# Performance work log

Hardware: AMD Instinct MI355X
Metric: run time of the kernel (lower is better)

The kernel has to match this reference:

```python
import jax, jax.numpy as jnp
import numpy as np

B, L, P, NH = 16384, 64, 2, 128
T = L // P          # number of patches (GRU steps)
NOUT = 1 << P       # softmax over 2**p possible patches


def setup_inputs() -> dict:
    key = jax.random.key(0)
    ks = jax.random.split(key, 10)
    s_in = 1.0 / np.sqrt(NH)
    x = jax.random.randint(ks[0], (B, L, 1), 0, 2).astype(jnp.float32)
    return {
        "x": x,
        # GRU params, torch layout: gates ordered (r, z, n)
        "w_ih": jax.random.normal(ks[1], (3 * NH, P), jnp.float32) * s_in,
        "w_hh": jax.random.normal(ks[2], (3 * NH, NH), jnp.float32) * s_in,
        "b_ih": jax.random.normal(ks[3], (3 * NH,), jnp.float32) * s_in,
        "b_hh": jax.random.normal(ks[4], (3 * NH,), jnp.float32) * s_in,
        # MLP head: Linear(Nh,Nh) -> ReLU -> Linear(Nh, 2**p) -> Softmax
        "w1": jax.random.normal(ks[5], (NH, NH), jnp.float32) * s_in,
        "b1": jax.random.normal(ks[6], (NH,), jnp.float32) * s_in,
        "w2": jax.random.normal(ks[7], (NOUT, NH), jnp.float32) * s_in,
        "b2": jax.random.normal(ks[8], (NOUT,), jnp.float32) * s_in,
    }


def _gru_mlp_logp(x, w_ih, w_hh, b_ih, b_hh, w1, b1, w2, b2):
    b = x.shape[0]
    patches = x.reshape(b, T, P)                       # Patch1D.forward
    # shift right by one patch (teacher forcing input), first step is zeros
    data = jnp.concatenate([jnp.zeros((b, 1, P), x.dtype), patches[:, :-1]], axis=1)
    # precompute all input-side gate projections: [B,T,3*Nh]
    xi = jnp.einsum('btp,gp->btg', data, w_ih) + b_ih

    def step(h, xi_t):
        gi_r, gi_z, gi_n = jnp.split(xi_t, 3, axis=-1)
        gh = h @ w_hh.T + b_hh
        gh_r, gh_z, gh_n = jnp.split(gh, 3, axis=-1)
        r = jax.nn.sigmoid(gi_r + gh_r)
        z = jax.nn.sigmoid(gi_z + gh_z)
        n = jnp.tanh(gi_n + r * gh_n)
        h_new = (1.0 - z) * n + z * h
        return h_new, h_new

    h0 = jnp.zeros((b, NH), x.dtype)
    _, hs = jax.lax.scan(step, h0, jnp.swapaxes(xi, 0, 1))  # [T,B,Nh]
    hs = jnp.swapaxes(hs, 0, 1)                              # [B,T,Nh]

    hid = jax.nn.relu(hs @ w1.T + b1)
    probs = jax.nn.softmax(hid @ w2.T + b2, axis=-1)         # [B,T,2**p]

    # genpatch2onehot: binary-encode each patch, little-endian (bit i -> 2**i)
    weights = (1 << jnp.arange(P)).astype(jnp.float32)
    idx = jnp.sum(patches * weights, axis=-1).astype(jnp.int32)  # [B,T]
    total = jnp.take_along_axis(probs, idx[..., None], axis=-1)[..., 0]
    return jnp.sum(jnp.log(total), axis=1)                   # [B]


def reference(x, w_ih, w_hh, b_ih, b_hh, w1, b1, w2, b2):
    return _gru_mlp_logp(x, w_ih, w_hh, b_ih, b_hh, w1, b1, w2, b2)
```

## Files before the change

kernel.cpp:

```cpp
#include <hip/hip_runtime.h>
#include <hip/hip_bf16.h>


#define NSTEP 32
#define BT    32
#define BLK   512

using s8v = __attribute__((ext_vector_type(8))) short;
using f4v = __attribute__((ext_vector_type(4))) float;

#define L2E 1.4426950408889634f
#define LN2 0.6931471805599453f

__device__ __forceinline__ unsigned short f2bf(float f) {
  __hip_bfloat16 h = __float2bfloat16(f);
  return __builtin_bit_cast(unsigned short, h);
}
__device__ __forceinline__ unsigned pkbf2(float a, float b) {
  return (unsigned)f2bf(a) | ((unsigned)f2bf(b) << 16);
}
__device__ __forceinline__ s8v pack8(float4 u, float4 v) {
  s8v a;
  a[0]=(short)f2bf(u.x); a[1]=(short)f2bf(u.y); a[2]=(short)f2bf(u.z); a[3]=(short)f2bf(u.w);
  a[4]=(short)f2bf(v.x); a[5]=(short)f2bf(v.y); a[6]=(short)f2bf(v.z); a[7]=(short)f2bf(v.w);
  return a;
}
__device__ __forceinline__ f4v mfma16(s8v a, s8v b, f4v c) {
  return __builtin_amdgcn_mfma_f32_16x16x32_bf16(a, b, c, 0, 0, 0);
}
__device__ __forceinline__ float sigm(float x) {
  return __builtin_amdgcn_rcpf(1.f + __builtin_amdgcn_exp2f(-L2E * x));
}
__device__ __forceinline__ float tanhc(float x) {
  return __builtin_fmaf(2.f, __builtin_amdgcn_rcpf(1.f + __builtin_amdgcn_exp2f((-2.f*L2E) * x)), -1.f);
}

__global__ __launch_bounds__(BLK, 4) void prnn_kernel(
    const float* __restrict__ x, const float* __restrict__ w_ih,
    const float* __restrict__ w_hh, const float* __restrict__ b_ih,
    const float* __restrict__ b_hh, const float* __restrict__ w1,
    const float* __restrict__ b1, const float* __restrict__ w2,
    const float* __restrict__ b2, float* __restrict__ out) {

  __shared__ __align__(16) unsigned char lds_h[4*2*64*16];
  __shared__ __align__(16) unsigned char lds_hid[4*2*64*16];
  __shared__ __align__(16) unsigned char lds_wA1[8*4*64*16];
  __shared__ __align__(16) unsigned char lds_w2f[4*64*16];
  __shared__ __align__(16) float lds_xrz[64*4*4];
  __shared__ __align__(16) float lds_xn[32*4*4];
  __shared__ __align__(16) float lds_bb[256];
  __shared__ __align__(16) float lds_b2[4];
  __shared__ unsigned lds_idx[32*8];
  __shared__ float lds_lp[8][32];

  const int tid = threadIdx.x;
  const int bbase = blockIdx.x * BT;
  const int lane = tid & 63;
  const int lg = lane >> 4, ln = lane & 15;
  const int w = __builtin_amdgcn_readfirstlane(tid >> 6);

  if (tid < 256) {
    int b = tid >> 3, ch = tid & 7;
    const float* xp = x + (size_t)(bbase + b) * 64 + ch * 8;
    float4 v0 = *(const float4*)xp, v1 = *(const float4*)(xp + 4);
    unsigned pk = ((v0.x!=0.f?1u:0u) | (v0.y!=0.f?2u:0u))
               | (((v0.z!=0.f?1u:0u) | (v0.w!=0.f?2u:0u)) << 8)
               | (((v1.x!=0.f?1u:0u) | (v1.y!=0.f?2u:0u)) << 16)
               | (((v1.z!=0.f?1u:0u) | (v1.w!=0.f?2u:0u)) << 24);
    lds_idx[b*8 + ch] = pk;
  }
  if (tid < 256) {
    int j = tid;
    float base = b_ih[j] + b_hh[j];
    float wa = w_ih[2*j], wb = w_ih[2*j+1];
    int q = j >> 2, e = j & 3;
    #pragma unroll
    for (int v = 0; v < 4; ++v)
      lds_xrz[(q*4+v)*4 + e] = base + ((v&1) ? wa : 0.f) + ((v&2) ? wb : 0.f);
  }
  if (tid < 128) {
    int j2 = 256 + tid;
    float bn = b_ih[j2];
    float wan = w_ih[2*j2], wbn = w_ih[2*j2+1];
    int qn = tid >> 2, en = tid & 3;
    #pragma unroll
    for (int v = 0; v < 4; ++v)
      lds_xn[(qn*4+v)*4 + en] = bn + ((v&1) ? wan : 0.f) + ((v&2) ? wbn : 0.f);
  }
  if (tid < 128) lds_bb[tid] = b_hh[256 + tid];
  else if (tid < 256) lds_bb[tid] = b1[tid - 128];
  if (tid < 4) lds_b2[tid] = b2[tid];
  #pragma unroll
  for (int it = 0; it < 4; ++it) {
    int i = tid + it * BLK;
    int mt = i >> 8, ks = (i >> 6) & 3, l = i & 63;
    const float* src = w1 + (16*mt + (l & 15)) * 128 + ks*32 + (l >> 4)*8;
    *(s8v*)(lds_wA1 + ((mt*4 + ks)*64 + l)*16) = pack8(*(const float4*)src, *(const float4*)(src+4));
  }
  if (tid < 256) {
    int ks = tid >> 6, l = tid & 63;
    s8v fr;
    #pragma unroll
    for (int e = 0; e < 8; ++e) fr[e] = (short)0;
    if ((l & 15) < 4) {
      const float* src = w2 + (l & 15) * 128 + ks*32 + (l >> 4)*8;
      fr = pack8(*(const float4*)src, *(const float4*)(src + 4));
    }
    *(s8v*)(lds_w2f + (ks*64 + l)*16) = fr;
  }

  s8v Ar[4], Az[4], An[4];
  {
    const int row = 16*w + ln;
    #pragma unroll
    for (int ks = 0; ks < 4; ++ks) {
      const float* s0 = w_hh + row*128 + ks*32 + lg*8;
      Ar[ks] = pack8(*(const float4*)s0, *(const float4*)(s0 + 4));
      const float* s1 = s0 + 128*128;
      Az[ks] = pack8(*(const float4*)s1, *(const float4*)(s1 + 4));
      const float* s2 = s0 + 256*128;
      An[ks] = pack8(*(const float4*)s2, *(const float4*)(s2 + 4));
    }
  }

  __syncthreads();

  unsigned pk0a=0, pk0b=0, pk1a=0, pk1b=0;
  #pragma unroll
  for (int w8 = 0; w8 < 4; ++w8) {
    unsigned u = lds_idx[ln*8 + w8];
    pk0a |= (((u&3u) | ((u>>6)&0xCu) | ((u>>12)&0x30u) | ((u>>18)&0xC0u)) << (8*w8));
    unsigned u2 = lds_idx[(16+ln)*8 + w8];
    pk1a |= (((u2&3u) | ((u2>>6)&0xCu) | ((u2>>12)&0x30u) | ((u2>>18)&0xC0u)) << (8*w8));
  }
  #pragma unroll
  for (int w8 = 4; w8 < 8; ++w8) {
    unsigned u = lds_idx[ln*8 + w8];
    pk0b |= (((u&3u) | ((u>>6)&0xCu) | ((u>>12)&0x30u) | ((u>>18)&0xC0u)) << (8*(w8-4)));
    unsigned u2 = lds_idx[(16+ln)*8 + w8];
    pk1b |= (((u2&3u) | ((u2>>6)&0xCu) | ((u2>>12)&0x30u) | ((u2>>18)&0xC0u)) << (8*(w8-4)));
  }

  const unsigned wroff = (unsigned)((((w>>1)*128) + 16*(2*(w&1) + (lg>>1)) + ln)*16 + 8*(lg&1));
  const int q = 4*w + lg;

  s8v Bf[4][2];
  #pragma unroll
  for (int ks = 0; ks < 4; ++ks)
    #pragma unroll
    for (int nt = 0; nt < 2; ++nt)
      #pragma unroll
      for (int e = 0; e < 8; ++e) Bf[ks][nt][e] = (short)0;
  f4v hfr[2];
  hfr[0][0]=0.f; hfr[0][1]=0.f; hfr[0][2]=0.f; hfr[0][3]=0.f;
  hfr[1] = hfr[0];
  float lp0 = 0.f, lp1 = 0.f;
  int pv0 = 0, pv1 = 0;

  for (int tb = 0; tb < NSTEP; tb += 8) {
    const unsigned pc0 = (tb & 16) ? pk0b : pk0a;
    const unsigned pc1 = (tb & 16) ? pk1b : pk1a;
    #pragma unroll
    for (int k = 0; k < 8; ++k) {
      const int t = tb + k;
      const f4v aNi = *(const f4v*)&lds_bb[q*4];
      #pragma unroll
      for (int nt = 0; nt < 2; ++nt) {
        const int var = nt ? pv1 : pv0;
        f4v aR = *(const f4v*)&lds_xrz[(q*4 + var)*4];
        f4v aZ = *(const f4v*)&lds_xrz[((q+32)*4 + var)*4];
        f4v aN = aNi;
        #pragma unroll
        for (int ks = 0; ks < 4; ++ks) {
          aR = mfma16(Ar[ks], Bf[ks][nt], aR);
          aZ = mfma16(Az[ks], Bf[ks][nt], aZ);
          aN = mfma16(An[ks], Bf[ks][nt], aN);
        }
        const f4v xnv = *(const f4v*)&lds_xn[(q*4 + var)*4];
        f4v hn;
        #pragma unroll
        for (int r = 0; r < 4; ++r) {
          float R  = sigm(aR[r]);
          float Z  = sigm(aZ[r]);
          float Ng = tanhc(__builtin_fmaf(R, aN[r], xnv[r]));
          hn[r] = __builtin_fmaf(Z, hfr[nt][r] - Ng, Ng);
        }
        hfr[nt] = hn;
        uint2 wv;
        wv.x = pkbf2(hn[0], hn[1]);
        wv.y = pkbf2(hn[2], hn[3]);
        *(uint2*)(lds_h + wroff + (unsigned)(nt*1024)) = wv;
      }
      __syncthreads();
      #pragma unroll
      for (int ks = 0; ks < 4; ++ks)
        #pragma unroll
        for (int nt = 0; nt < 2; ++nt)
          Bf[ks][nt] = *(const s8v*)(lds_h + ((ks*2 + nt)*64 + lane)*16);
      const f4v b1i = *(const f4v*)&lds_bb[128 + q*4];
      f4v hc0 = b1i, hc1 = b1i;
      #pragma unroll
      for (int ks = 0; ks < 4; ++ks) {
        const s8v wf = *(const s8v*)(lds_wA1 + ((w*4 + ks)*64 + lane)*16);
        hc0 = mfma16(wf, Bf[ks][0], hc0);
        hc1 = mfma16(wf, Bf[ks][1], hc1);
      }
      {
        uint2 wv;
        wv.x = pkbf2(fmaxf(hc0[0],0.f), fmaxf(hc0[1],0.f));
        wv.y = pkbf2(fmaxf(hc0[2],0.f), fmaxf(hc0[3],0.f));
        *(uint2*)(lds_hid + wroff) = wv;
        wv.x = pkbf2(fmaxf(hc1[0],0.f), fmaxf(hc1[1],0.f));
        wv.y = pkbf2(fmaxf(hc1[2],0.f), fmaxf(hc1[3],0.f));
        *(uint2*)(lds_hid + wroff + 1024u) = wv;
      }
      __syncthreads();
      const int sh  = (2*t) & 31;
      const int ic0 = (int)((pc0 >> sh) & 3);
      const int ic1 = (int)((pc1 >> sh) & 3);
      if (w == k) {
        const f4v b2v = *(const f4v*)lds_b2;
        f4v la0, la1;
        #pragma unroll
        for (int r = 0; r < 4; ++r) {
          la0[r] = (lg == 0) ? b2v[r] : 0.f;
          la1[r] = la0[r];
        }
        #pragma unroll
        for (int ks = 0; ks < 4; ++ks) {
          const s8v W2f = *(const s8v*)(lds_w2f + (ks*64 + lane)*16);
          la0 = mfma16(W2f, *(const s8v*)(lds_hid + ((ks*2 + 0)*64 + lane)*16), la0);
          la1 = mfma16(W2f, *(const s8v*)(lds_hid + ((ks*2 + 1)*64 + lane)*16), la1);
        }
        if (lg == 0) {
          {
            float l0=la0[0], l1=la0[1], l2=la0[2], l3=la0[3];
            float m = fmaxf(fmaxf(l0, l1), fmaxf(l2, l3));
            float s = __builtin_amdgcn_exp2f((l0-m)*L2E) + __builtin_amdgcn_exp2f((l1-m)*L2E)
                    + __builtin_amdgcn_exp2f((l2-m)*L2E) + __builtin_amdgcn_exp2f((l3-m)*L2E);
            float sel = (ic0 == 0) ? l0 : (ic0 == 1) ? l1 : (ic0 == 2) ? l2 : l3;
            lp0 += (sel - m) - __builtin_amdgcn_logf(s) * LN2;
          }
          {
            float l0=la1[0], l1=la1[1], l2=la1[2], l3=la1[3];
            float m = fmaxf(fmaxf(l0, l1), fmaxf(l2, l3));
            float s = __builtin_amdgcn_exp2f((l0-m)*L2E) + __builtin_amdgcn_exp2f((l1-m)*L2E)
                    + __builtin_amdgcn_exp2f((l2-m)*L2E) + __builtin_amdgcn_exp2f((l3-m)*L2E);
            float sel = (ic1 == 0) ? l0 : (ic1 == 1) ? l1 : (ic1 == 2) ? l2 : l3;
            lp1 += (sel - m) - __builtin_amdgcn_logf(s) * LN2;
          }
        }
      }
      pv0 = ic0; pv1 = ic1;
    }
  }

  if (lg == 0) { lds_lp[w][ln] = lp0; lds_lp[w][16 + ln] = lp1; }
  __syncthreads();
  if (tid < 32) {
    float s = 0.f;
    #pragma unroll
    for (int ww = 0; ww < 8; ++ww) s += lds_lp[ww][tid];
    out[bbase + tid] = s;
  }
}

extern "C" void kernel_launch(void* const* d_in, const int* in_sizes, int n_in,
                              void* d_out, int out_size, void* d_ws, size_t ws_size,
                              hipStream_t stream) {
  const float* x    = (const float*)d_in[0];
  const float* w_ih = (const float*)d_in[1];
  const float* w_hh = (const float*)d_in[2];
  const float* b_ih = (const float*)d_in[3];
  const float* b_hh = (const float*)d_in[4];
  const float* w1   = (const float*)d_in[5];
  const float* b1   = (const float*)d_in[6];
  const float* w2   = (const float*)d_in[7];
  const float* b2   = (const float*)d_in[8];
  float* out = (float*)d_out;
  int B = in_sizes[0] / 64;
  int grid = B / BT;
  prnn_kernel<<<grid, BLK, 0, stream>>>(x, w_ih, w_hh, b_ih, b_hh, w1, b1, w2, b2, out);
}
```

Before: 100.0 us.

## Double-buffer GRU hidden/MLP LDS to drop a barrier and defer the output head

```diff
diff --git a/kernel.cpp b/kernel.cpp
--- a/kernel.cpp
+++ b/kernel.cpp
@@ -19,20 +19,20 @@
 __device__ __forceinline__ unsigned pkbf2(float a, float b) {
   return (unsigned)f2bf(a) | ((unsigned)f2bf(b) << 16);
 }
-__device__ __forceinline__ s8v pack8(float4 u, float4 v) {
+__device__ __forceinline__ s8v pack8s(float sc, float4 u, float4 v) {
   s8v a;
-  a[0]=(short)f2bf(u.x); a[1]=(short)f2bf(u.y); a[2]=(short)f2bf(u.z); a[3]=(short)f2bf(u.w);
-  a[4]=(short)f2bf(v.x); a[5]=(short)f2bf(v.y); a[6]=(short)f2bf(v.z); a[7]=(short)f2bf(v.w);
+  a[0]=(short)f2bf(sc*u.x); a[1]=(short)f2bf(sc*u.y); a[2]=(short)f2bf(sc*u.z); a[3]=(short)f2bf(sc*u.w);
+  a[4]=(short)f2bf(sc*v.x); a[5]=(short)f2bf(sc*v.y); a[6]=(short)f2bf(sc*v.z); a[7]=(short)f2bf(sc*v.w);
   return a;
 }
 __device__ __forceinline__ f4v mfma16(s8v a, s8v b, f4v c) {
   return __builtin_amdgcn_mfma_f32_16x16x32_bf16(a, b, c, 0, 0, 0);
 }
-__device__ __forceinline__ float sigm(float x) {
-  return __builtin_amdgcn_rcpf(1.f + __builtin_amdgcn_exp2f(-L2E * x));
-}
-__device__ __forceinline__ float tanhc(float x) {
-  return __builtin_fmaf(2.f, __builtin_amdgcn_rcpf(1.f + __builtin_amdgcn_exp2f((-2.f*L2E) * x)), -1.f);
+__device__ __forceinline__ float sigm2(float x) {
+  return __builtin_amdgcn_rcpf(1.f + __builtin_amdgcn_exp2f(-x));
+}
+__device__ __forceinline__ float tanh2(float x) {
+  return __builtin_fmaf(2.f, __builtin_amdgcn_rcpf(1.f + __builtin_amdgcn_exp2f(-x)), -1.f);
 }
 
 __global__ __launch_bounds__(BLK, 4) void prnn_kernel(
@@ -42,14 +42,12 @@
     const float* __restrict__ b1, const float* __restrict__ w2,
     const float* __restrict__ b2, float* __restrict__ out) {
 
-  __shared__ __align__(16) unsigned char lds_h[4*2*64*16];
-  __shared__ __align__(16) unsigned char lds_hid[4*2*64*16];
+  __shared__ __align__(16) unsigned char lds_h[2][8192];
+  __shared__ __align__(16) unsigned char lds_hid[2][8192];
   __shared__ __align__(16) unsigned char lds_wA1[8*4*64*16];
   __shared__ __align__(16) unsigned char lds_w2f[4*64*16];
   __shared__ __align__(16) float lds_xrz[64*4*4];
   __shared__ __align__(16) float lds_xn[32*4*4];
-  __shared__ __align__(16) float lds_bb[256];
-  __shared__ __align__(16) float lds_b2[4];
   __shared__ unsigned lds_idx[32*8];
   __shared__ float lds_lp[8][32];
 
@@ -76,7 +74,7 @@
     int q = j >> 2, e = j & 3;
     #pragma unroll
     for (int v = 0; v < 4; ++v)
-      lds_xrz[(q*4+v)*4 + e] = base + ((v&1) ? wa : 0.f) + ((v&2) ? wb : 0.f);
+      lds_xrz[(q*4+v)*4 + e] = L2E * (base + ((v&1) ? wa : 0.f) + ((v&2) ? wb : 0.f));
   }
   if (tid < 128) {
     int j2 = 256 + tid;
@@ -85,17 +83,14 @@
     int qn = tid >> 2, en = tid & 3;
     #pragma unroll
     for (int v = 0; v < 4; ++v)
-      lds_xn[(qn*4+v)*4 + en] = bn + ((v&1) ? wan : 0.f) + ((v&2) ? wbn : 0.f);
-  }
-  if (tid < 128) lds_bb[tid] = b_hh[256 + tid];
-  else if (tid < 256) lds_bb[tid] = b1[tid - 128];
-  if (tid < 4) lds_b2[tid] = b2[tid];
+      lds_xn[(qn*4+v)*4 + en] = (2.f*L2E) * (bn + ((v&1) ? wan : 0.f) + ((v&2) ? wbn : 0.f));
+  }
   #pragma unroll
   for (int it = 0; it < 4; ++it) {
     int i = tid + it * BLK;
     int mt = i >> 8, ks = (i >> 6) & 3, l = i & 63;
     const float* src = w1 + (16*mt + (l & 15)) * 128 + ks*32 + (l >> 4)*8;
-    *(s8v*)(lds_wA1 + ((mt*4 + ks)*64 + l)*16) = pack8(*(const float4*)src, *(const float4*)(src+4));
+    *(s8v*)(lds_wA1 + ((mt*4 + ks)*64 + l)*16) = pack8s(1.f, *(const float4*)src, *(const float4*)(src+4));
   }
   if (tid < 256) {
     int ks = tid >> 6, l = tid & 63;
@@ -104,7 +99,7 @@
     for (int e = 0; e < 8; ++e) fr[e] = (short)0;
     if ((l & 15) < 4) {
       const float* src = w2 + (l & 15) * 128 + ks*32 + (l >> 4)*8;
-      fr = pack8(*(const float4*)src, *(const float4*)(src + 4));
+      fr = pack8s(1.f, *(const float4*)src, *(const float4*)(src + 4));
     }
     *(s8v*)(lds_w2f + (ks*64 + l)*16) = fr;
   }
@@ -115,12 +110,21 @@
     #pragma unroll
     for (int ks = 0; ks < 4; ++ks) {
       const float* s0 = w_hh + row*128 + ks*32 + lg*8;
-      Ar[ks] = pack8(*(const float4*)s0, *(const float4*)(s0 + 4));
+      Ar[ks] = pack8s(L2E, *(const float4*)s0, *(const float4*)(s0 + 4));
       const float* s1 = s0 + 128*128;
-      Az[ks] = pack8(*(const float4*)s1, *(const float4*)(s1 + 4));
+      Az[ks] = pack8s(L2E, *(const float4*)s1, *(const float4*)(s1 + 4));
       const float* s2 = s0 + 256*128;
-      An[ks] = pack8(*(const float4*)s2, *(const float4*)(s2 + 4));
-    }
+      An[ks] = pack8s(2.f*L2E, *(const float4*)s2, *(const float4*)(s2 + 4));
+    }
+  }
+  const int q = 4*w + lg;
+  f4v bhnr, b1i, b2r;
+  {
+    const f4v bh = *(const f4v*)(b_hh + 256 + q*4);
+    bhnr[0]=(2.f*L2E)*bh[0]; bhnr[1]=(2.f*L2E)*bh[1]; bhnr[2]=(2.f*L2E)*bh[2]; bhnr[3]=(2.f*L2E)*bh[3];
+    b1i = *(const f4v*)(b1 + q*4);
+    if (lg == 0) b2r = *(const f4v*)b2;
+    else { b2r[0]=0.f; b2r[1]=0.f; b2r[2]=0.f; b2r[3]=0.f; }
   }
 
   __syncthreads();
@@ -142,7 +146,6 @@
   }
 
   const unsigned wroff = (unsigned)((((w>>1)*128) + 16*(2*(w&1) + (lg>>1)) + ln)*16 + 8*(lg&1));
-  const int q = 4*w + lg;
 
   s8v Bf[4][2];
   #pragma unroll
@@ -157,19 +160,43 @@
   float lp0 = 0.f, lp1 = 0.f;
   int pv0 = 0, pv1 = 0;
 
+  auto do_p5 = [&](int u, int uslot) {
+    const int ua = u & 7;
+    const bool d0 = (w == ua), d1 = (w == (ua ^ 4));
+    if (d0 | d1) {
+      const int ntx = d1 ? 1 : 0;
+      f4v la = b2r;
+      #pragma unroll
+      for (int ks = 0; ks < 4; ++ks) {
+        const s8v W2f = *(const s8v*)(lds_w2f + (ks*64 + lane)*16);
+        const s8v Bh  = *(const s8v*)(&lds_hid[uslot][((ks*2 + ntx)*64 + lane)*16]);
+        la = mfma16(W2f, Bh, la);
+      }
+      if (lg == 0) {
+        const unsigned hsel = ntx ? ((u & 16) ? pk1b : pk1a) : ((u & 16) ? pk0b : pk0a);
+        const int ic = (int)((hsel >> ((2*u) & 31)) & 3);
+        float l0=la[0], l1=la[1], l2=la[2], l3=la[3];
+        float m = fmaxf(fmaxf(l0, l1), fmaxf(l2, l3));
+        float s = __builtin_amdgcn_exp2f((l0-m)*L2E) + __builtin_amdgcn_exp2f((l1-m)*L2E)
+                + __builtin_amdgcn_exp2f((l2-m)*L2E) + __builtin_amdgcn_exp2f((l3-m)*L2E);
+        float sel = (ic == 0) ? l0 : (ic == 1) ? l1 : (ic == 2) ? l2 : l3;
+        float v = (sel - m) - __builtin_amdgcn_logf(s) * LN2;
+        if (ntx) lp1 += v; else lp0 += v;
+      }
+    }
+  };
+
   for (int tb = 0; tb < NSTEP; tb += 8) {
-    const unsigned pc0 = (tb & 16) ? pk0b : pk0a;
-    const unsigned pc1 = (tb & 16) ? pk1b : pk1a;
     #pragma unroll
     for (int k = 0; k < 8; ++k) {
       const int t = tb + k;
-      const f4v aNi = *(const f4v*)&lds_bb[q*4];
+      const int slot = t & 1;
       #pragma unroll
       for (int nt = 0; nt < 2; ++nt) {
         const int var = nt ? pv1 : pv0;
         f4v aR = *(const f4v*)&lds_xrz[(q*4 + var)*4];
         f4v aZ = *(const f4v*)&lds_xrz[((q+32)*4 + var)*4];
-        f4v aN = aNi;
+        f4v aN = bhnr;
         #pragma unroll
         for (int ks = 0; ks < 4; ++ks) {
           aR = mfma16(Ar[ks], Bf[ks][nt], aR);
@@ -180,24 +207,23 @@
         f4v hn;
         #pragma unroll
         for (int r = 0; r < 4; ++r) {
-          float R  = sigm(aR[r]);
-          float Z  = sigm(aZ[r]);
-          float Ng = tanhc(__builtin_fmaf(R, aN[r], xnv[r]));
+          float R  = sigm2(aR[r]);
+          float Z  = sigm2(aZ[r]);
+          float Ng = tanh2(__builtin_fmaf(R, aN[r], xnv[r]));
           hn[r] = __builtin_fmaf(Z, hfr[nt][r] - Ng, Ng);
         }
         hfr[nt] = hn;
         uint2 wv;
         wv.x = pkbf2(hn[0], hn[1]);
         wv.y = pkbf2(hn[2], hn[3]);
-        *(uint2*)(lds_h + wroff + (unsigned)(nt*1024)) = wv;
+        *(uint2*)(&lds_h[slot][wroff + (unsigned)(nt*1024)]) = wv;
       }
       __syncthreads();
       #pragma unroll
       for (int ks = 0; ks < 4; ++ks)
         #pragma unroll
         for (int nt = 0; nt < 2; ++nt)
-          Bf[ks][nt] = *(const s8v*)(lds_h + ((ks*2 + nt)*64 + lane)*16);
-      const f4v b1i = *(const f4v*)&lds_bb[128 + q*4];
+          Bf[ks][nt] = *(const s8v*)(&lds_h[slot][((ks*2 + nt)*64 + lane)*16]);
       f4v hc0 = b1i, hc1 = b1i;
       #pragma unroll
       for (int ks = 0; ks < 4; ++ks) {
@@ -209,51 +235,24 @@
         uint2 wv;
         wv.x = pkbf2(fmaxf(hc0[0],0.f), fmaxf(hc0[1],0.f));
         wv.y = pkbf2(fmaxf(hc0[2],0.f), fmaxf(hc0[3],0.f));
-        *(uint2*)(lds_hid + wroff) = wv;
+        *(uint2*)(&lds_hid[slot][wroff]) = wv;
         wv.x = pkbf2(fmaxf(hc1[0],0.f), fmaxf(hc1[1],0.f));
         wv.y = pkbf2(fmaxf(hc1[2],0.f), fmaxf(hc1[3],0.f));
-        *(uint2*)(lds_hid + wroff + 1024u) = wv;
-      }
-      __syncthreads();
-      const int sh  = (2*t) & 31;
-      const int ic0 = (int)((pc0 >> sh) & 3);
-      const int ic1 = (int)((pc1 >> sh) & 3);
-      if (w == k) {
-        const f4v b2v = *(const f4v*)lds_b2;
-        f4v la0, la1;
-        #pragma unroll
-        for (int r = 0; r < 4; ++r) {
-          la0[r] = (lg == 0) ? b2v[r] : 0.f;
-          la1[r] = la0[r];
-        }
-        #pragma unroll
-        for (int ks = 0; ks < 4; ++ks) {
-          const s8v W2f = *(const s8v*)(lds_w2f + (ks*64 + lane)*16);
-          la0 = mfma16(W2f, *(const s8v*)(lds_hid + ((ks*2 + 0)*64 + lane)*16), la0);
-          la1 = mfma16(W2f, *(const s8v*)(lds_hid + ((ks*2 + 1)*64 + lane)*16), la1);
-        }
-        if (lg == 0) {
-          {
-            float l0=la0[0], l1=la0[1], l2=la0[2], l3=la0[3];
-            float m = fmaxf(fmaxf(l0, l1), fmaxf(l2, l3));
-            float s = __builtin_amdgcn_exp2f((l0-m)*L2E) + __builtin_amdgcn_exp2f((l1-m)*L2E)
-                    + __builtin_amdgcn_exp2f((l2-m)*L2E) + __builtin_amdgcn_exp2f((l3-m)*L2E);
-            float sel = (ic0 == 0) ? l0 : (ic0 == 1) ? l1 : (ic0 == 2) ? l2 : l3;
-            lp0 += (sel - m) - __builtin_amdgcn_logf(s) * LN2;
-          }
-          {
-            float l0=la1[0], l1=la1[1], l2=la1[2], l3=la1[3];
-            float m = fmaxf(fmaxf(l0, l1), fmaxf(l2, l3));
-            float s = __builtin_amdgcn_exp2f((l0-m)*L2E) + __builtin_amdgcn_exp2f((l1-m)*L2E)
-                    + __builtin_amdgcn_exp2f((l2-m)*L2E) + __builtin_amdgcn_exp2f((l3-m)*L2E);
-            float sel = (ic1 == 0) ? l0 : (ic1 == 1) ? l1 : (ic1 == 2) ? l2 : l3;
-            lp1 += (sel - m) - __builtin_amdgcn_logf(s) * LN2;
-          }
-        }
-      }
-      pv0 = ic0; pv1 = ic1;
-    }
-  }
+        *(uint2*)(&lds_hid[slot][wroff + 1024u]) = wv;
+      }
+      if (t > 0) do_p5(t - 1, slot ^ 1);
+      {
+        const unsigned g0 = (t & 16) ? pk0b : pk0a;
+        const unsigned g1 = (t & 16) ? pk1b : pk1a;
+        const int sh = (2*t) & 31;
+        pv0 = (int)((g0 >> sh) & 3);
+        pv1 = (int)((g1 >> sh) & 3);
+      }
+    }
+  }
+
+  __syncthreads();
+  do_p5(NSTEP - 1, (NSTEP - 1) & 1);
 
   if (lg == 0) { lds_lp[w][ln] = lp0; lds_lp[w][16 + ln] = lp1; }
   __syncthreads();
```

After: 113.9 us. 13.8% more time.
